# Kernel optimization log

Hardware: AMD Instinct MI355X
Metric: run time of the kernel (lower is better)

## Reference

```python
import jax, jax.numpy as jnp
import numpy as np
from jax import lax

EPS = 1e-5
DN = ('NCDHW', 'OIDHW', 'NCDHW')


def _instance_norm(x, w, b):
    # normalize over spatial dims per (batch, channel); biased variance like torch
    mu = jnp.mean(x, axis=(2, 3, 4), keepdims=True)
    var = jnp.mean((x - mu) ** 2, axis=(2, 3, 4), keepdims=True)
    xn = (x - mu) * lax.rsqrt(var + EPS)
    return xn * w[None, :, None, None, None] + b[None, :, None, None, None]


def _conv1x1(x, w, b):
    # w: [Cout, Cin]
    y = jnp.einsum('bcdhw,oc->bodhw', x, w)
    return y + b[None, :, None, None, None]


def _dwconv3(x, w, b):
    # depthwise 3x3x3, padding 1; w: [C, 1, 3, 3, 3]
    y = lax.conv_general_dilated(x, w, (1, 1, 1), 'SAME',
                                 dimension_numbers=DN,
                                 feature_group_count=w.shape[0])
    return y + b[None, :, None, None, None]


def setup_inputs() -> dict:
    key = jax.random.key(0)
    ks = jax.random.split(key, 8)
    C, half = 64, 32
    B, D, H, W = 1, 96, 96, 96
    s1 = 1.0 / np.sqrt(C)          # fan_in of 1x1 conv
    s3 = 1.0 / np.sqrt(27.0)       # fan_in of depthwise 3x3x3
    return {
        'x': jax.random.normal(ks[0], (B, C, D, H, W), jnp.float32),
        'norm_w': jnp.ones((C,), jnp.float32),
        'norm_b': jnp.zeros((C,), jnp.float32),
        'in_proj_w': jax.random.normal(ks[1], (C, C), jnp.float32) * s1,
        'in_proj_b': jnp.zeros((C,), jnp.float32),
        'conv_ssm_w': jax.random.normal(ks[2], (half, 1, 3, 3, 3), jnp.float32) * s3,
        'conv_ssm_b': jnp.zeros((half,), jnp.float32),
        'mamba_w': jax.random.normal(ks[3], (half, 1, 3, 3, 3), jnp.float32) * s3,
        'mamba_b': jnp.zeros((half,), jnp.float32),
        'conv_sym_w': jax.random.normal(ks[4], (half, 1, 3, 3, 3), jnp.float32) * s3,
        'conv_sym_b': jnp.zeros((half,), jnp.float32),
        'out_proj_w': jax.random.normal(ks[5], (C, C), jnp.float32) * s1,
        'out_proj_b': jnp.zeros((C,), jnp.float32),
    }


def reference(x, norm_w, norm_b, in_proj_w, in_proj_b,
              conv_ssm_w, conv_ssm_b, mamba_w, mamba_b,
              conv_sym_w, conv_sym_b, out_proj_w, out_proj_b):
    residual = x
    xp = _conv1x1(_instance_norm(x, norm_w, norm_b), in_proj_w, in_proj_b)
    half = xp.shape[1] // 2
    x1, x2 = xp[:, :half], xp[:, half:]
    # SSM branch (TriDirectionalMamba fallback = depthwise conv3)
    x1 = _dwconv3(jax.nn.silu(_dwconv3(x1, conv_ssm_w, conv_ssm_b)), mamba_w, mamba_b)
    # symmetric conv branch
    x2 = jax.nn.silu(_dwconv3(x2, conv_sym_w, conv_sym_b))
    y = _conv1x1(jnp.concatenate([x1, x2], axis=1), out_proj_w, out_proj_b)
    return y + residual
```

## Files before the change

### kernel.cpp

```cpp
#include <hip/hip_runtime.h>

typedef unsigned short u16;
typedef unsigned int u32;
typedef short bf16x8 __attribute__((ext_vector_type(8)));
typedef float f32x16 __attribute__((ext_vector_type(16)));
typedef u16 u16x8 __attribute__((ext_vector_type(8)));

#define DIM 96
#define PLANE (DIM*DIM)
#define S 884736
#define C 64
#define HALF 32
#define PARTS 16
#define EPS 1e-5f
#define DSPLIT 4
#define DCHUNK (DIM/DSPLIT)

#define RPADF 108
#define LROWS 18
#define LBUFF (LROWS*RPADF)

#define MFMA32(a,b,c) __builtin_amdgcn_mfma_f32_32x32x16_bf16(a,b,c,0,0,0)

__device__ __forceinline__ u16 f2bf(float f) {
  u32 u = __builtin_bit_cast(u32, f);
  return (u16)((u + 0x7FFFu + ((u >> 16) & 1u)) >> 16);
}
__device__ __forceinline__ float bf2f(u16 h) {
  return __builtin_bit_cast(float, (u32)h << 16);
}
__device__ __forceinline__ u32 cvt_pk_bf16(float lo, float hi) {
  u32 r;
  asm("v_cvt_pk_bf16_f32 %0, %1, %2" : "=v"(r) : "v"(lo), "v"(hi));
  return r;
}
__device__ __forceinline__ float silu(float v) { return v / (1.f + __expf(-v)); }
__device__ __forceinline__ u16x8 zero8() {
  u16x8 z;
  #pragma unroll
  for (int i = 0; i < 8; ++i) z[i] = 0;
  return z;
}

__global__ __launch_bounds__(256) void k1_stats(const float* __restrict__ x,
                                                u16* __restrict__ xb,
                                                float* __restrict__ psum,
                                                float* __restrict__ psq) {
  const int bid = blockIdx.x;
  const int ch = bid / PARTS, part = bid % PARTS;
  const int chunk = S / PARTS;
  const size_t base = (size_t)ch * S + (size_t)part * chunk;
  const float4* p = (const float4*)(x + base);
  ushort4* xb4 = (ushort4*)(xb + base);
  const int n4 = chunk / 4;
  float s = 0.f, q = 0.f;
  for (int i = threadIdx.x; i < n4; i += 256) {
    float4 v = p[i];
    s += (v.x + v.y) + (v.z + v.w);
    q += (v.x * v.x + v.y * v.y) + (v.z * v.z + v.w * v.w);
    union { u32 u[2]; ushort4 v4; } o;
    o.u[0] = cvt_pk_bf16(v.x, v.y);
    o.u[1] = cvt_pk_bf16(v.z, v.w);
    xb4[i] = o.v4;
  }
  #pragma unroll
  for (int off = 32; off > 0; off >>= 1) {
    s += __shfl_down(s, off);
    q += __shfl_down(q, off);
  }
  __shared__ float ls[4], lq[4];
  const int wid = threadIdx.x >> 6, lane = threadIdx.x & 63;
  if (lane == 0) { ls[wid] = s; lq[wid] = q; }
  __syncthreads();
  if (threadIdx.x == 0) {
    psum[bid] = (ls[0] + ls[1]) + (ls[2] + ls[3]);
    psq[bid]  = (lq[0] + lq[1]) + (lq[2] + lq[3]);
  }
}

__global__ __launch_bounds__(64) void k1b_prep(const float* __restrict__ psum,
    const float* __restrict__ psq,
    const float* __restrict__ norm_w, const float* __restrict__ norm_b,
    const float* __restrict__ in_w, const float* __restrict__ in_b,
    const float* __restrict__ out_w,
    u16* __restrict__ Wp, float* __restrict__ biasp, u16* __restrict__ Wo) {
  __shared__ float a_s[C], b2_s[C];
  const int t = threadIdx.x;
  float s = 0.f, q = 0.f;
  for (int i = 0; i < PARTS; ++i) { s += psum[t * PARTS + i]; q += psq[t * PARTS + i]; }
  const float inv = 1.f / (float)S;
  const float mu = s * inv;
  const float var = q * inv - mu * mu;
  const float rsig = rsqrtf(var + EPS);
  const float a = norm_w[t] * rsig;
  const float b2 = norm_b[t] - mu * a;
  a_s[t] = a; b2_s[t] = b2;
  __syncthreads();
  float bp = in_b[t];
  for (int c = 0; c < C; ++c) {
    const float w = in_w[t * C + c];
    Wp[t * C + c] = f2bf(w * a_s[c]);
    bp += b2_s[c] * w;
    Wo[t * C + c] = f2bf(out_w[t * C + c]);
  }
  biasp[t] = bp;
}

__global__ __launch_bounds__(256) void k2_mfma(const u16* __restrict__ xb,
    const u16* __restrict__ Wp, const float* __restrict__ biasp,
    u16* __restrict__ xp) {
  const int lane = threadIdx.x & 63, wid = threadIdx.x >> 6;
  const int n = lane & 31, hf = lane >> 5;
  const int v0 = blockIdx.x * 256 + wid * 64;
  bf16x8 A[2][4];
  #pragma unroll
  for (int t = 0; t < 2; ++t)
    #pragma unroll
    for (int s = 0; s < 4; ++s)
      A[t][s] = *(const bf16x8*)(Wp + (t * 32 + n) * C + s * 16 + hf * 8);

  f32x16 accE[2], accO[2];
  #pragma unroll
  for (int t = 0; t < 2; ++t)
    #pragma unroll
    for (int r = 0; r < 16; ++r) {
      const float b = biasp[t * 32 + (r & 3) + 8 * (r >> 2) + 4 * hf];
      accE[t][r] = b; accO[t][r] = b;
    }

  #pragma unroll
  for (int s = 0; s < 4; ++s) {
    union { u16 u[8]; bf16x8 v; } BE, BO;
    #pragma unroll
    for (int j = 0; j < 8; ++j) {
      const u32 xv = *(const u32*)(xb + (size_t)(s * 16 + hf * 8 + j) * S + v0 + 2 * n);
      BE.u[j] = (u16)(xv & 0xFFFFu); BO.u[j] = (u16)(xv >> 16);
    }
    #pragma unroll
    for (int t = 0; t < 2; ++t) {
      accE[t] = MFMA32(A[t][s], BE.v, accE[t]);
      accO[t] = MFMA32(A[t][s], BO.v, accO[t]);
    }
  }
  #pragma unroll
  for (int t = 0; t < 2; ++t)
    #pragma unroll
    for (int r = 0; r < 16; ++r) {
      const int o = t * 32 + (r & 3) + 8 * (r >> 2) + 4 * hf;
      *(u32*)(xp + (size_t)o * S + v0 + 2 * n) = cvt_pk_bf16(accE[t][r], accO[t][r]);
    }
}

__device__ __forceinline__ void fma3(float* __restrict__ a,
    const float* __restrict__ r, float t0, float t1, float t2) {
  #pragma unroll
  for (int i = 0; i < 8; ++i) a[i] = fmaf(t0, r[i], a[i]);
  #pragma unroll
  for (int i = 0; i < 8; ++i) a[i] = fmaf(t1, r[i + 1], a[i]);
  #pragma unroll
  for (int i = 0; i < 8; ++i) a[i] = fmaf(t2, r[i + 2], a[i]);
}

template<bool SILU>
__global__ __launch_bounds__(192) void dwconv(const u16* __restrict__ srcA,
    const float* __restrict__ kwA, const float* __restrict__ bA,
    u16* __restrict__ dstA,
    const float* __restrict__ kwB, const float* __restrict__ bB,
    u16* __restrict__ dstB) {
  __shared__ float lds[2][LBUFF];
  const int c = blockIdx.z;
  const u16* src = srcA + (size_t)c * S;
  u16* dst; const float* kwp; float bias;
  if (c < HALF) { dst = dstA + (size_t)c * S;          kwp = kwA + c * 27;          bias = bA[c]; }
  else          { dst = dstB + (size_t)(c - HALF) * S; kwp = kwB + (c - HALF) * 27; bias = bB[c - HALF]; }
  float kw[27];
  #pragma unroll
  for (int i = 0; i < 27; ++i) kw[i] = kwp[i];

  const int tx = threadIdx.x, ty = threadIdx.y;
  const int tid = ty * 12 + tx;
  const int w8 = tx * 8;
  const int h0 = blockIdx.x * 16;
  const int d0 = blockIdx.y * DCHUNK;

  if (tid < 36) {
    const int b = tid / 18, r = tid % 18;
    float4 z4 = make_float4(0.f, 0.f, 0.f, 0.f);
    *(float4*)&lds[b][r * RPADF + 0] = z4;
    *(float4*)&lds[b][r * RPADF + 4] = z4;
    *(float4*)&lds[b][r * RPADF + 104] = z4;
  }

  const int s_row0 = tid / 12, s_cc0 = tid % 12;
  const int s_row1 = (192 + tid) / 12, s_cc1 = (192 + tid) % 12;
  const bool has2 = tid < 24;
  const int s_h0 = h0 - 1 + s_row0;
  const int s_h1 = h0 - 1 + s_row1;
  const bool h0ok = (unsigned)s_h0 < DIM;
  const bool h1ok = has2 && ((unsigned)s_h1 < DIM);
  u16x8 vs0, vs1;

  #define STAGE_LOAD(DD) { \
    vs0 = zero8(); vs1 = zero8(); \
    if (((unsigned)(DD) < DIM) && h0ok) \
      vs0 = *(const u16x8*)(src + (size_t)(DD) * PLANE + s_h0 * DIM + s_cc0 * 8); \
    if (((unsigned)(DD) < DIM) && h1ok) \
      vs1 = *(const u16x8*)(src + (size_t)(DD) * PLANE + s_h1 * DIM + s_cc1 * 8); }

  #define STAGE_WRITE(WB) { \
    float4 f0, f1; \
    f0.x = bf2f(vs0[0]); f0.y = bf2f(vs0[1]); f0.z = bf2f(vs0[2]); f0.w = bf2f(vs0[3]); \
    f1.x = bf2f(vs0[4]); f1.y = bf2f(vs0[5]); f1.z = bf2f(vs0[6]); f1.w = bf2f(vs0[7]); \
    *(float4*)&lds[WB][8 + s_row0 * RPADF + s_cc0 * 8] = f0; \
    *(float4*)&lds[WB][8 + s_row0 * RPADF + s_cc0 * 8 + 4] = f1; \
    if (has2) { \
      f0.x = bf2f(vs1[0]); f0.y = bf2f(vs1[1]); f0.z = bf2f(vs1[2]); f0.w = bf2f(vs1[3]); \
      f1.x = bf2f(vs1[4]); f1.y = bf2f(vs1[5]); f1.z = bf2f(vs1[6]); f1.w = bf2f(vs1[7]); \
      *(float4*)&lds[WB][8 + s_row1 * RPADF + s_cc1 * 8] = f0; \
      *(float4*)&lds[WB][8 + s_row1 * RPADF + s_cc1 * 8 + 4] = f1; } }

  float r0[10], r1[10], r2[10];
  float A[8], B[8], o8[8];

  #define LOADROW(R, ROWI, RB) { \
    const float* _lb = &lds[RB][8 + (ROWI) * RPADF + w8]; \
    const float4 _a = *(const float4*)_lb; \
    const float4 _b = *(const float4*)(_lb + 4); \
    R[0] = _lb[-1]; \
    R[1] = _a.x; R[2] = _a.y; R[3] = _a.z; R[4] = _a.w; \
    R[5] = _b.x; R[6] = _b.y; R[7] = _b.z; R[8] = _b.w; \
    R[9] = _lb[8]; }

  #define LOADROWS(RB) { LOADROW(r0, ty, RB); LOADROW(r1, ty + 1, RB); LOADROW(r2, ty + 2, RB); }

  #define CBLK(ACC, K0) { \
    fma3(ACC, r0, kw[(K0) + 0], kw[(K0) + 1], kw[(K0) + 2]); \
    fma3(ACC, r1, kw[(K0) + 3], kw[(K0) + 4], kw[(K0) + 5]); \
    fma3(ACC, r2, kw[(K0) + 6], kw[(K0) + 7], kw[(K0) + 8]); }

  STAGE_LOAD(d0 - 1);
  STAGE_WRITE(0);
  __syncthreads();

  LOADROWS(0);
  STAGE_LOAD(d0);
  #pragma unroll
  for (int i = 0; i < 8; ++i) B[i] = bias;
  CBLK(B, 0);
  STAGE_WRITE(1);
  __syncthreads();

  LOADROWS(1);
  STAGE_LOAD(d0 + 1);
  #pragma unroll
  for (int i = 0; i < 8; ++i) { A[i] = B[i]; B[i] = bias; }
  CBLK(A, 9);
  CBLK(B, 0);
  STAGE_WRITE(0);
  __syncthreads();

  u16* db = dst + (size_t)d0 * PLANE + (size_t)(h0 + ty) * DIM + w8;

  #define ROUND_BODY(D, RB, WB, DO_STG) { \
    if (DO_STG) STAGE_LOAD((D) + 2); \
    LOADROWS(RB); \
    _Pragma("unroll") \
    for (int i = 0; i < 8; ++i) o8[i] = A[i]; \
    CBLK(o8, 18); \
    _Pragma("unroll") \
    for (int i = 0; i < 8; ++i) A[i] = B[i]; \
    CBLK(A, 9); \
    _Pragma("unroll") \
    for (int i = 0; i < 8; ++i) B[i] = bias; \
    CBLK(B, 0); \
    if (SILU) { \
      _Pragma("unroll") \
      for (int i = 0; i < 8; ++i) o8[i] = silu(o8[i]); \
    } \
    union { u32 u[4]; u16x8 v; } _o; \
    _Pragma("unroll") \
    for (int i = 0; i < 4; ++i) _o.u[i] = cvt_pk_bf16(o8[2 * i], o8[2 * i + 1]); \
    *(u16x8*)db = _o.v; \
    db += PLANE; \
    if (DO_STG) STAGE_WRITE(WB); \
    __syncthreads(); }

  #pragma unroll 1
  for (int d = d0; d < d0 + DCHUNK; d += 2) {
    ROUND_BODY(d, 0, 1, true);
    ROUND_BODY(d + 1, 1, 0, (d + 2) < d0 + DCHUNK);
  }
  #undef ROUND_BODY
  #undef CBLK
  #undef LOADROWS
  #undef LOADROW
  #undef STAGE_WRITE
  #undef STAGE_LOAD
}

__global__ __launch_bounds__(256) void k4b_mfma(const u16* __restrict__ z_lo,
    const u16* __restrict__ z_hi, const u16* __restrict__ xb,
    const u16* __restrict__ Wo, const float* __restrict__ ob,
    float* __restrict__ out) {
  const int lane = threadIdx.x & 63, wid = threadIdx.x >> 6;
  const int n = lane & 31, hf = lane >> 5;
  const int v0 = blockIdx.x * 256 + wid * 64;
  bf16x8 A[2][4];
  #pragma unroll
  for (int t = 0; t < 2; ++t)
    #pragma unroll
    for (int s = 0; s < 4; ++s)
      A[t][s] = *(const bf16x8*)(Wo + (t * 32 + n) * C + s * 16 + hf * 8);

  f32x16 accE[2], accO[2];
  #pragma unroll
  for (int t = 0; t < 2; ++t)
    #pragma unroll
    for (int r = 0; r < 16; ++r) {
      const float b = ob[t * 32 + (r & 3) + 8 * (r >> 2) + 4 * hf];
      accE[t][r] = b; accO[t][r] = b;
    }

  #pragma unroll
  for (int s = 0; s < 4; ++s) {
    const u16* zbase = (s < 2) ? z_lo + (size_t)(s * 16) * S
                               : z_hi + (size_t)((s - 2) * 16) * S;
    union { u16 u[8]; bf16x8 v; } BE, BO;
    #pragma unroll
    for (int j = 0; j < 8; ++j) {
      const u32 zv = *(const u32*)(zbase + (size_t)(hf * 8 + j) * S + v0 + 2 * n);
      BE.u[j] = (u16)(zv & 0xFFFFu); BO.u[j] = (u16)(zv >> 16);
    }
    #pragma unroll
    for (int t = 0; t < 2; ++t) {
      accE[t] = MFMA32(A[t][s], BE.v, accE[t]);
      accO[t] = MFMA32(A[t][s], BO.v, accO[t]);
    }
  }
  #pragma unroll
  for (int t = 0; t < 2; ++t)
    #pragma unroll
    for (int r = 0; r < 16; ++r) {
      const int o = t * 32 + (r & 3) + 8 * (r >> 2) + 4 * hf;
      const u32 xr = *(const u32*)(xb + (size_t)o * S + v0 + 2 * n);
      float2 ov;
      ov.x = accE[t][r] + bf2f((u16)(xr & 0xFFFFu));
      ov.y = accO[t][r] + bf2f((u16)(xr >> 16));
      *(float2*)(out + (size_t)o * S + v0 + 2 * n) = ov;
    }
}

extern "C" void kernel_launch(void* const* d_in, const int* in_sizes, int n_in,
                              void* d_out, int out_size, void* d_ws, size_t ws_size,
                              hipStream_t stream) {
  const float* x      = (const float*)d_in[0];
  const float* norm_w = (const float*)d_in[1];
  const float* norm_b = (const float*)d_in[2];
  const float* in_w   = (const float*)d_in[3];
  const float* in_b   = (const float*)d_in[4];
  const float* ssm_w  = (const float*)d_in[5];
  const float* ssm_b  = (const float*)d_in[6];
  const float* mam_w  = (const float*)d_in[7];
  const float* mam_b  = (const float*)d_in[8];
  const float* sym_w  = (const float*)d_in[9];
  const float* sym_b  = (const float*)d_in[10];
  const float* out_w  = (const float*)d_in[11];
  const float* out_b  = (const float*)d_in[12];
  float* out = (float*)d_out;

  u16* xb   = (u16*)d_ws;
  u16* xp   = xb + (size_t)C * S;
  u16* t1   = xp + (size_t)C * S;
  u16* z_hi = t1 + (size_t)HALF * S;
  u16* z_lo = xp;
  float* psum  = (float*)(z_hi + (size_t)HALF * S);
  float* psq   = psum + C * PARTS;
  u16* Wp      = (u16*)(psq + C * PARTS);
  u16* Wo      = Wp + C * C;
  float* biasp = (float*)(Wo + C * C);

  k1_stats<<<C * PARTS, 256, 0, stream>>>(x, xb, psum, psq);
  k1b_prep<<<1, 64, 0, stream>>>(psum, psq, norm_w, norm_b, in_w, in_b, out_w,
                                 Wp, biasp, Wo);
  k2_mfma<<<S / 256, 256, 0, stream>>>(xb, Wp, biasp, xp);
  dwconv<true><<<dim3(DIM / 16, DSPLIT, C), dim3(12, 16, 1), 0, stream>>>(
      xp, ssm_w, ssm_b, t1, sym_w, sym_b, z_hi);
  dwconv<false><<<dim3(DIM / 16, DSPLIT, HALF), dim3(12, 16, 1), 0, stream>>>(
      t1, mam_w, mam_b, z_lo, mam_w, mam_b, z_lo);
  k4b_mfma<<<S / 256, 256, 0, stream>>>(z_lo, z_hi, xb, Wo, out_b, out);
}
```

Before: 370.3 us.

## Stage two depth planes per barrier in depthwise conv pipeline

The depthwise 3x3x3 conv kernel now loads and stages two depth planes per round into a double-buffered LDS array holding two planes per buffer. Each round computes two output planes between barriers, halving the number of __syncthreads calls and giving more global loads in flight per round. In exchange LDS use per block doubles and registers rise from holding four staged vectors, which may reduce occupancy.

```diff
diff --git a/kernel.cpp b/kernel.cpp
--- a/kernel.cpp
+++ b/kernel.cpp
@@ -167,7 +167,7 @@
     u16* __restrict__ dstA,
     const float* __restrict__ kwB, const float* __restrict__ bB,
     u16* __restrict__ dstB) {
-  __shared__ float lds[2][LBUFF];
+  __shared__ float lds[2][2][LBUFF];
   const int c = blockIdx.z;
   const u16* src = srcA + (size_t)c * S;
   u16* dst; const float* kwp; float bias;
@@ -183,12 +183,12 @@
   const int h0 = blockIdx.x * 16;
   const int d0 = blockIdx.y * DCHUNK;
 
-  if (tid < 36) {
-    const int b = tid / 18, r = tid % 18;
-    float4 z4 = make_float4(0.f, 0.f, 0.f, 0.f);
-    *(float4*)&lds[b][r * RPADF + 0] = z4;
-    *(float4*)&lds[b][r * RPADF + 4] = z4;
-    *(float4*)&lds[b][r * RPADF + 104] = z4;
+  if (tid < 72) {
+    float* rowp = &lds[tid / 36][(tid / 18) & 1][(tid % 18) * RPADF];
+    const float4 z4 = make_float4(0.f, 0.f, 0.f, 0.f);
+    *(float4*)&rowp[0] = z4;
+    *(float4*)&rowp[4] = z4;
+    *(float4*)&rowp[104] = z4;
   }
 
   const int s_row0 = tid / 12, s_cc0 = tid % 12;
@@ -198,32 +198,34 @@
   const int s_h1 = h0 - 1 + s_row1;
   const bool h0ok = (unsigned)s_h0 < DIM;
   const bool h1ok = has2 && ((unsigned)s_h1 < DIM);
-  u16x8 vs0, vs1;
-
-  #define STAGE_LOAD(DD) { \
-    vs0 = zero8(); vs1 = zero8(); \
-    if (((unsigned)(DD) < DIM) && h0ok) \
-      vs0 = *(const u16x8*)(src + (size_t)(DD) * PLANE + s_h0 * DIM + s_cc0 * 8); \
-    if (((unsigned)(DD) < DIM) && h1ok) \
-      vs1 = *(const u16x8*)(src + (size_t)(DD) * PLANE + s_h1 * DIM + s_cc1 * 8); }
-
-  #define STAGE_WRITE(WB) { \
+  u16x8 vA0, vA1, vB0, vB1;
+
+  #define LD8(DD, HH, CC) (*(const u16x8*)(src + (size_t)(DD) * PLANE + (HH) * DIM + (CC) * 8))
+
+  #define STAGE_LOAD2(D1, D2) { \
+    vA0 = zero8(); vA1 = zero8(); vB0 = zero8(); vB1 = zero8(); \
+    if (((unsigned)(D1) < DIM) && h0ok) vA0 = LD8(D1, s_h0, s_cc0); \
+    if (((unsigned)(D1) < DIM) && h1ok) vA1 = LD8(D1, s_h1, s_cc1); \
+    if (((unsigned)(D2) < DIM) && h0ok) vB0 = LD8(D2, s_h0, s_cc0); \
+    if (((unsigned)(D2) < DIM) && h1ok) vB1 = LD8(D2, s_h1, s_cc1); }
+
+  #define WR8(P, SL, ROW, CC, V) { \
     float4 f0, f1; \
-    f0.x = bf2f(vs0[0]); f0.y = bf2f(vs0[1]); f0.z = bf2f(vs0[2]); f0.w = bf2f(vs0[3]); \
-    f1.x = bf2f(vs0[4]); f1.y = bf2f(vs0[5]); f1.z = bf2f(vs0[6]); f1.w = bf2f(vs0[7]); \
-    *(float4*)&lds[WB][8 + s_row0 * RPADF + s_cc0 * 8] = f0; \
-    *(float4*)&lds[WB][8 + s_row0 * RPADF + s_cc0 * 8 + 4] = f1; \
-    if (has2) { \
-      f0.x = bf2f(vs1[0]); f0.y = bf2f(vs1[1]); f0.z = bf2f(vs1[2]); f0.w = bf2f(vs1[3]); \
-      f1.x = bf2f(vs1[4]); f1.y = bf2f(vs1[5]); f1.z = bf2f(vs1[6]); f1.w = bf2f(vs1[7]); \
-      *(float4*)&lds[WB][8 + s_row1 * RPADF + s_cc1 * 8] = f0; \
-      *(float4*)&lds[WB][8 + s_row1 * RPADF + s_cc1 * 8 + 4] = f1; } }
+    f0.x = bf2f(V[0]); f0.y = bf2f(V[1]); f0.z = bf2f(V[2]); f0.w = bf2f(V[3]); \
+    f1.x = bf2f(V[4]); f1.y = bf2f(V[5]); f1.z = bf2f(V[6]); f1.w = bf2f(V[7]); \
+    *(float4*)&lds[P][SL][8 + (ROW) * RPADF + (CC) * 8] = f0; \
+    *(float4*)&lds[P][SL][8 + (ROW) * RPADF + (CC) * 8 + 4] = f1; }
+
+  #define STAGE_WRITE2(P) { \
+    WR8(P, 0, s_row0, s_cc0, vA0); \
+    WR8(P, 1, s_row0, s_cc0, vB0); \
+    if (has2) { WR8(P, 0, s_row1, s_cc1, vA1); WR8(P, 1, s_row1, s_cc1, vB1); } }
 
   float r0[10], r1[10], r2[10];
   float A[8], B[8], o8[8];
 
-  #define LOADROW(R, ROWI, RB) { \
-    const float* _lb = &lds[RB][8 + (ROWI) * RPADF + w8]; \
+  #define LOADROW(R, ROWI, P, SL) { \
+    const float* _lb = &lds[P][SL][8 + (ROWI) * RPADF + w8]; \
     const float4 _a = *(const float4*)_lb; \
     const float4 _b = *(const float4*)(_lb + 4); \
     R[0] = _lb[-1]; \
@@ -231,39 +233,17 @@
     R[5] = _b.x; R[6] = _b.y; R[7] = _b.z; R[8] = _b.w; \
     R[9] = _lb[8]; }
 
-  #define LOADROWS(RB) { LOADROW(r0, ty, RB); LOADROW(r1, ty + 1, RB); LOADROW(r2, ty + 2, RB); }
+  #define LOADROWS(P, SL) { LOADROW(r0, ty, P, SL); LOADROW(r1, ty + 1, P, SL); LOADROW(r2, ty + 2, P, SL); }
 
   #define CBLK(ACC, K0) { \
     fma3(ACC, r0, kw[(K0) + 0], kw[(K0) + 1], kw[(K0) + 2]); \
     fma3(ACC, r1, kw[(K0) + 3], kw[(K0) + 4], kw[(K0) + 5]); \
     fma3(ACC, r2, kw[(K0) + 6], kw[(K0) + 7], kw[(K0) + 8]); }
 
-  STAGE_LOAD(d0 - 1);
-  STAGE_WRITE(0);
-  __syncthreads();
-
-  LOADROWS(0);
-  STAGE_LOAD(d0);
-  #pragma unroll
-  for (int i = 0; i < 8; ++i) B[i] = bias;
-  CBLK(B, 0);
-  STAGE_WRITE(1);
-  __syncthreads();
-
-  LOADROWS(1);
-  STAGE_LOAD(d0 + 1);
-  #pragma unroll
-  for (int i = 0; i < 8; ++i) { A[i] = B[i]; B[i] = bias; }
-  CBLK(A, 9);
-  CBLK(B, 0);
-  STAGE_WRITE(0);
-  __syncthreads();
-
   u16* db = dst + (size_t)d0 * PLANE + (size_t)(h0 + ty) * DIM + w8;
 
-  #define ROUND_BODY(D, RB, WB, DO_STG) { \
-    if (DO_STG) STAGE_LOAD((D) + 2); \
-    LOADROWS(RB); \
+  #define CSTEP(P, SL) { \
+    LOADROWS(P, SL); \
     _Pragma("unroll") \
     for (int i = 0; i < 8; ++i) o8[i] = A[i]; \
     CBLK(o8, 18); \
@@ -281,21 +261,47 @@
     _Pragma("unroll") \
     for (int i = 0; i < 4; ++i) _o.u[i] = cvt_pk_bf16(o8[2 * i], o8[2 * i + 1]); \
     *(u16x8*)db = _o.v; \
-    db += PLANE; \
-    if (DO_STG) STAGE_WRITE(WB); \
+    db += PLANE; }
+
+  STAGE_LOAD2(d0 - 1, d0);
+  STAGE_WRITE2(1);
+  __syncthreads();
+
+  LOADROWS(1, 0);
+  #pragma unroll
+  for (int i = 0; i < 8; ++i) B[i] = bias;
+  CBLK(B, 0);
+  LOADROWS(1, 1);
+  #pragma unroll
+  for (int i = 0; i < 8; ++i) { A[i] = B[i]; B[i] = bias; }
+  CBLK(A, 9);
+  CBLK(B, 0);
+  STAGE_LOAD2(d0 + 1, d0 + 2);
+  STAGE_WRITE2(0);
+  __syncthreads();
+
+  #define ROUND(R, P, DO_STG) { \
+    if (DO_STG) STAGE_LOAD2((R) + 3, (R) + 4); \
+    CSTEP(P, 0); \
+    CSTEP(P, 1); \
+    if (DO_STG) STAGE_WRITE2(P ^ 1); \
     __syncthreads(); }
 
   #pragma unroll 1
-  for (int d = d0; d < d0 + DCHUNK; d += 2) {
-    ROUND_BODY(d, 0, 1, true);
-    ROUND_BODY(d + 1, 1, 0, (d + 2) < d0 + DCHUNK);
-  }
-  #undef ROUND_BODY
+  for (int it = 0; it < DCHUNK / 4; ++it) {
+    const int r = d0 + 4 * it;
+    ROUND(r, 0, true);
+    ROUND(r + 2, 1, (4 * it + 4) < DCHUNK);
+  }
+  #undef ROUND
+  #undef CSTEP
   #undef CBLK
   #undef LOADROWS
   #undef LOADROW
-  #undef STAGE_WRITE
-  #undef STAGE_LOAD
+  #undef STAGE_WRITE2
+  #undef WR8
+  #undef STAGE_LOAD2
+  #undef LD8
 }
 
 __global__ __launch_bounds__(256) void k4b_mfma(const u16* __restrict__ z_lo,
```

After: 362.9 us. -2.0%, faster.
